# Kernel tuning notes

Measured on AMD Instinct MI355X. Metric: run time of the kernel, lower is better.

## Reference

```python
import jax, jax.numpy as jnp
import numpy as np

N = 100000      # nodes
E = 1600000     # directed edges (avg degree 16)
D_IN = 64
D_OUT = 64


def setup_inputs() -> dict:
    key = jax.random.key(0)
    k1, k2, k3, k4, k5 = jax.random.split(key, 5)
    x = jax.random.normal(k1, (N, D_IN), dtype=jnp.float32)
    edge_index = jax.random.randint(k2, (2, E), 0, N, dtype=jnp.int32)
    s_in = 1.0 / np.sqrt(D_IN)
    W_conv = jax.random.normal(k3, (D_IN, D_OUT), dtype=jnp.float32) * s_in
    b_conv = jnp.zeros((D_OUT,), dtype=jnp.float32)
    W_self = jax.random.normal(k4, (D_IN, D_OUT), dtype=jnp.float32) * s_in
    b_self = jax.random.normal(k5, (D_OUT,), dtype=jnp.float32) * s_in
    return {"x": x, "edge_index": edge_index, "W_conv": W_conv, "b_conv": b_conv,
            "W_self": W_self, "b_self": b_self, "n1": 400, "n2": 250}


def reference(x, edge_index, W_conv, b_conv, W_self, b_self, n1, n2):
    # GCNConv (PyG defaults): add self-loops, symmetric normalization,
    # out_i = sum_j norm_ij * (x_j @ W_conv) + b_conv; then self-loop linear + residual.
    n = x.shape[0]
    loops = jnp.arange(n, dtype=edge_index.dtype)
    row = jnp.concatenate([edge_index[0], loops])  # source nodes [E+N]
    col = jnp.concatenate([edge_index[1], loops])  # target nodes [E+N]
    deg = jax.ops.segment_sum(jnp.ones_like(col, dtype=x.dtype), col, num_segments=n)
    dinv = jnp.where(deg > 0, jax.lax.rsqrt(deg), 0.0)      # deg^{-1/2}
    norm = dinv[row] * dinv[col]                            # [E+N]
    xw = x @ W_conv                                         # [N, D_OUT]
    msg = xw[row] * norm[:, None]                           # gather + scale [E+N, D_OUT]
    x_neigh = jax.ops.segment_sum(msg, col, num_segments=n) + b_conv
    x_self = x @ W_self + b_self
    return x_self + x_neigh
```

## Files before the change

kernel.cpp:

```cpp
#include <hip/hip_runtime.h>

#define CAP 64
#define CHUNK 4096
#define NBINS_MAX 1024
#define CAPB 2560

typedef __attribute__((ext_vector_type(8))) short bf16x8;
typedef __attribute__((ext_vector_type(4))) float f32x4;

__device__ __forceinline__ unsigned short f2bf_rne(float f) {
    unsigned u = __builtin_bit_cast(unsigned, f);
    u += 0x7FFFu + ((u >> 16) & 1u);
    return (unsigned short)(u >> 16);
}
__device__ __forceinline__ float bf2f(unsigned short h) {
    return __builtin_bit_cast(float, (unsigned)h << 16);
}


__global__ void k_zero2(int* __restrict__ gcur, int nbins, int* __restrict__ degovf,
                        int n, int* __restrict__ ovfc,
                        const float* __restrict__ Wc, const float* __restrict__ Ws,
                        unsigned short* __restrict__ bfrag) {
    const int t = threadIdx.x;
    if (blockIdx.x == gridDim.x - 1) {
        for (int s = t; s < 2048; s += 256) {
            int lane = s & 63;
            int ct   = (s >> 6) & 3;
            int ks   = (s >> 8) & 1;
            int half = (s >> 9) & 1;
            int mat  = (s >> 10) & 1;
            const float* W = mat ? Ws : Wc;
            int d = ct * 16 + (lane & 15);
            int kbase = ks * 32 + (lane >> 4) * 8;
#pragma unroll
            for (int j = 0; j < 8; ++j) {
                float v = W[(kbase + j) * 64 + d];
                unsigned u = __builtin_bit_cast(unsigned, v);
                unsigned short hi = (unsigned short)(u >> 16);
                unsigned short elem;
                if (half == 0) {
                    elem = hi;
                } else {
                    float fh = __builtin_bit_cast(float, (unsigned)hi << 16);
                    float fl = v - fh;
                    elem = (unsigned short)(__builtin_bit_cast(unsigned, fl) >> 16);
                }
                bfrag[(size_t)s * 8 + j] = elem;
            }
        }
        return;
    }
    int i = blockIdx.x * blockDim.x + t;
    if (i < nbins) gcur[i] = 0;
    if (i < n) degovf[i] = 0;
    if (i == 0) *ovfc = 0;
}

__global__ __launch_bounds__(512) void k_bin(
    const int* __restrict__ row, const int* __restrict__ col, int e, int nbins,
    int* __restrict__ gcur, unsigned int* __restrict__ records,
    int* __restrict__ degovf, int* __restrict__ ovf, int* __restrict__ ovfc)
{
    __shared__ int hist[NBINS_MAX];
    __shared__ int lofs[NBINS_MAX];
    __shared__ int gadj[NBINS_MAX];
    __shared__ int tscan[512];
    __shared__ unsigned int stage[CHUNK];
    __shared__ unsigned short sbin[CHUNK];

    const int t = threadIdx.x;
    const int base = blockIdx.x * CHUNK;
    int cnt = e - base; if (cnt > CHUNK) cnt = CHUNK;
    if (cnt <= 0) return;

    for (int i = t; i < nbins; i += 512) hist[i] = 0;
    __syncthreads();

    for (int k = t; k < cnt; k += 512) atomicAdd(&hist[col[base + k] >> 7], 1);
    __syncthreads();

    const int b0 = t * 2;
    int h0 = (b0 < nbins) ? hist[b0] : 0;
    int h1 = (b0 + 1 < nbins) ? hist[b0 + 1] : 0;
    int s = h0 + h1;
    tscan[t] = s;
    __syncthreads();
    for (int off = 1; off < 512; off <<= 1) {
        int v = (t >= off) ? tscan[t - off] : 0;
        __syncthreads();
        tscan[t] += v;
        __syncthreads();
    }
    const int tbase = tscan[t] - s;

    if (b0 < nbins) {
        int gb = h0 ? atomicAdd(&gcur[b0], h0) : 0;
        lofs[b0] = tbase; gadj[b0] = gb - tbase;
    }
    if (b0 + 1 < nbins) {
        int lb = tbase + h0;
        int gb = h1 ? atomicAdd(&gcur[b0 + 1], h1) : 0;
        lofs[b0 + 1] = lb; gadj[b0 + 1] = gb - lb;
    }
    __syncthreads();

    for (int k = t; k < cnt; k += 512) {
        int c = col[base + k];
        int r = row[base + k];
        int b = c >> 7;
        int slot = atomicAdd(&lofs[b], 1);
        stage[slot] = ((unsigned)r << 7) | (unsigned)(c & 127);
        sbin[slot] = (unsigned short)b;
    }
    __syncthreads();

    for (int k = t; k < cnt; k += 512) {
        unsigned rec = stage[k];
        int b = sbin[k];
        int g = gadj[b] + k;
        if (g < CAPB) {
            records[(size_t)b * CAPB + g] = rec;
        } else {
            int q = atomicAdd(ovfc, 1);
            int c = (b << 7) | (int)(rec & 127u);
            ovf[2 * q]     = (int)(rec >> 7);
            ovf[2 * q + 1] = c;
            atomicAdd(&degovf[c], 1);
        }
    }
}

__global__ __launch_bounds__(256) void k_gemm6(
    const float* __restrict__ x, const unsigned short* __restrict__ bfrag,
    const float* __restrict__ bc, const float* __restrict__ bs,
    const unsigned int* __restrict__ records, const int* __restrict__ gcur,
    const int* __restrict__ degovf, float* __restrict__ dinv,
    unsigned short* __restrict__ ybf, float* __restrict__ out, int n)
{
    __shared__ int lh[128];
    __shared__ float sdinv[128];

    const int b = blockIdx.x;
    const int t = threadIdx.x;

    if (t < 128) lh[t] = 0;
    __syncthreads();
    int m = gcur[b]; if (m > CAPB) m = CAPB;
    const unsigned int* rb = records + (size_t)b * CAPB;
    for (int k = t; k < m; k += 256) atomicAdd(&lh[rb[k] & 127u], 1);
    __syncthreads();
    if (t < 128) {
        int node = (b << 7) + t;
        int dov = (node < n) ? degovf[node] : 0;
        float v = rsqrtf((float)(lh[t] + dov + 1));
        sdinv[t] = v;
        if (node < n) dinv[node] = v;
    }
    __syncthreads();

    const int lane = t & 63;
    const int wid = t >> 6;
    const int rt0 = b * 128 + wid * 32;
    const int lbase = wid * 32;
    if (rt0 >= n) return;

    const int arow = lane & 15;
    const int kgrp = lane >> 4;

    bf16x8 a_hi[2][2];
#pragma unroll
    for (int rt = 0; rt < 2; ++rt) {
        int row = rt0 + rt * 16 + arow;
        if (row >= n) row = n - 1;
        const float* xp = x + (size_t)row * 64 + kgrp * 8;
#pragma unroll
        for (int ks = 0; ks < 2; ++ks) {
            float4 f0 = *(const float4*)(xp + ks * 32);
            float4 f1 = *(const float4*)(xp + ks * 32 + 4);
            float f[8] = {f0.x, f0.y, f0.z, f0.w, f1.x, f1.y, f1.z, f1.w};
            bf16x8 h;
#pragma unroll
            for (int j = 0; j < 8; ++j) {
                unsigned u = __builtin_bit_cast(unsigned, f[j]);
                h[j] = (short)(unsigned short)(u >> 16);
            }
            a_hi[rt][ks] = h;
        }
    }

    f32x4 acc[2][2][4];
#pragma unroll
    for (int mm = 0; mm < 2; ++mm)
#pragma unroll
        for (int rt = 0; rt < 2; ++rt)
#pragma unroll
            for (int ct = 0; ct < 4; ++ct)
                acc[mm][rt][ct] = (f32x4){0.f, 0.f, 0.f, 0.f};

#pragma unroll
    for (int mat = 0; mat < 2; ++mat) {
#pragma unroll
        for (int ks = 0; ks < 2; ++ks) {
#pragma unroll
            for (int ct = 0; ct < 4; ++ct) {
                const bf16x8 bh = *(const bf16x8*)(bfrag + ((size_t)((((mat * 2 + 0) * 2 + ks) * 4 + ct) * 64 + lane)) * 8);
                const bf16x8 bl = *(const bf16x8*)(bfrag + ((size_t)((((mat * 2 + 1) * 2 + ks) * 4 + ct) * 64 + lane)) * 8);
#pragma unroll
                for (int rt = 0; rt < 2; ++rt) {
                    acc[mat][rt][ct] = __builtin_amdgcn_mfma_f32_16x16x32_bf16(a_hi[rt][ks], bh, acc[mat][rt][ct], 0, 0, 0);
                    acc[mat][rt][ct] = __builtin_amdgcn_mfma_f32_16x16x32_bf16(a_hi[rt][ks], bl, acc[mat][rt][ct], 0, 0, 0);
                }
            }
        }
    }

    const int dcol = lane & 15;
    const int rbase = (lane >> 4) * 4;
    float di[2][4];
#pragma unroll
    for (int rt = 0; rt < 2; ++rt)
#pragma unroll
        for (int reg = 0; reg < 4; ++reg)
            di[rt][reg] = sdinv[lbase + rt * 16 + rbase + reg];

#pragma unroll
    for (int ct = 0; ct < 4; ++ct) {
        int d = ct * 16 + dcol;
        float bias = bc[d] + bs[d];
#pragma unroll
        for (int rt = 0; rt < 2; ++rt) {
#pragma unroll
            for (int reg = 0; reg < 4; ++reg) {
                int row = rt0 + rt * 16 + rbase + reg;
                if (row < n) {
                    float dv = di[rt][reg];
                    float zc = acc[0][rt][ct][reg];
                    ybf[(size_t)row * 64 + d] = f2bf_rne(zc * dv);
                    out[(size_t)row * 64 + d] = acc[1][rt][ct][reg] + bias + dv * dv * zc;
                }
            }
        }
    }
}

__global__ __launch_bounds__(512) void k_gather_bin4(
    const int* __restrict__ gcur, const unsigned int* __restrict__ records,
    const unsigned short* __restrict__ ybf, const float* __restrict__ dinv,
    float* __restrict__ out, int n)
{
    __shared__ unsigned int srec[CAPB];
    __shared__ int slist[CAPB];
    __shared__ int scnt[128];
    __shared__ int sinc[128];
    __shared__ int scur[128];

    const int b = blockIdx.x, t = threadIdx.x;
    int m = gcur[b]; if (m > CAPB) m = CAPB;

    if (t < 128) scnt[t] = 0;
    __syncthreads();

    for (int k = t; k < m; k += 512) {
        unsigned r = __builtin_nontemporal_load(&records[(size_t)b * CAPB + k]);
        srec[k] = r;
        atomicAdd(&scnt[r & 127u], 1);
    }
    __syncthreads();

    if (t < 128) sinc[t] = scnt[t];
    __syncthreads();
    for (int off = 1; off < 128; off <<= 1) {
        int v = 0;
        if (t < 128 && t >= off) v = sinc[t - off];
        __syncthreads();
        if (t < 128) sinc[t] += v;
        __syncthreads();
    }
    if (t < 128) scur[t] = sinc[t] - scnt[t];
    __syncthreads();

    for (int k = t; k < m; k += 512) {
        unsigned r = srec[k];
        int slot = atomicAdd(&scur[r & 127u], 1);
        slist[slot] = (int)(r & ~127u);
    }
    __syncthreads();

    const int wave = t >> 6, lane = t & 63;
    const int h = lane >> 5;
    const char* ybl = (const char*)ybf + ((lane & 31) << 2);

    for (int i = wave; i < 128; i += 8) {
        int node = (b << 7) + i;
        if (node >= n) break;
        int cnt = scnt[i];
        if (cnt == 0) continue;
        int beg = sinc[i] - cnt;
        float ax0=0.f,ax1=0.f,ax2=0.f,ax3=0.f,ax4=0.f,ax5=0.f,ax6=0.f,ax7=0.f;
        float ay0=0.f,ay1=0.f,ay2=0.f,ay3=0.f,ay4=0.f,ay5=0.f,ay6=0.f,ay7=0.f;
        int k = 0;
        for (; k + 16 <= cnt; k += 16) {
            int o0 = slist[beg + k + 0  + h];
            int o1 = slist[beg + k + 2  + h];
            int o2 = slist[beg + k + 4  + h];
            int o3 = slist[beg + k + 6  + h];
            int o4 = slist[beg + k + 8  + h];
            int o5 = slist[beg + k + 10 + h];
            int o6 = slist[beg + k + 12 + h];
            int o7 = slist[beg + k + 14 + h];
            unsigned v0 = *(const unsigned*)(ybl + o0);
            unsigned v1 = *(const unsigned*)(ybl + o1);
            unsigned v2 = *(const unsigned*)(ybl + o2);
            unsigned v3 = *(const unsigned*)(ybl + o3);
            unsigned v4 = *(const unsigned*)(ybl + o4);
            unsigned v5 = *(const unsigned*)(ybl + o5);
            unsigned v6 = *(const unsigned*)(ybl + o6);
            unsigned v7 = *(const unsigned*)(ybl + o7);
            ax0 += bf2f((unsigned short)v0); ay0 += bf2f((unsigned short)(v0 >> 16));
            ax1 += bf2f((unsigned short)v1); ay1 += bf2f((unsigned short)(v1 >> 16));
            ax2 += bf2f((unsigned short)v2); ay2 += bf2f((unsigned short)(v2 >> 16));
            ax3 += bf2f((unsigned short)v3); ay3 += bf2f((unsigned short)(v3 >> 16));
            ax4 += bf2f((unsigned short)v4); ay4 += bf2f((unsigned short)(v4 >> 16));
            ax5 += bf2f((unsigned short)v5); ay5 += bf2f((unsigned short)(v5 >> 16));
            ax6 += bf2f((unsigned short)v6); ay6 += bf2f((unsigned short)(v6 >> 16));
            ax7 += bf2f((unsigned short)v7); ay7 += bf2f((unsigned short)(v7 >> 16));
        }
        for (; k + 2 <= cnt; k += 2) {
            int o = slist[beg + k + h];
            unsigned v = *(const unsigned*)(ybl + o);
            ax0 += bf2f((unsigned short)v);
            ay0 += bf2f((unsigned short)(v >> 16));
        }
        if (k < cnt && h == 0) {
            int o = slist[beg + k];
            unsigned v = *(const unsigned*)(ybl + o);
            ax0 += bf2f((unsigned short)v);
            ay0 += bf2f((unsigned short)(v >> 16));
        }
        float sx = ((ax0+ax1)+(ax2+ax3)) + ((ax4+ax5)+(ax6+ax7));
        float sy = ((ay0+ay1)+(ay2+ay3)) + ((ay4+ay5)+(ay6+ay7));
        sx += __shfl_down(sx, 32);
        sy += __shfl_down(sy, 32);
        if (h == 0) {
            float dv = dinv[node];
            float* op = out + (size_t)node * 64 + ((lane & 31) << 1);
            float p0 = __builtin_nontemporal_load(op);
            float p1 = __builtin_nontemporal_load(op + 1);
            __builtin_nontemporal_store(p0 + dv * sx, op);
            __builtin_nontemporal_store(p1 + dv * sy, op + 1);
        }
    }
}

__global__ void k_ovf2(const int* __restrict__ ovfc, const int* __restrict__ ovf,
                       const float* __restrict__ dinv, const unsigned short* __restrict__ ybf,
                       float* __restrict__ out) {
    int m = *ovfc;
    long long total = (long long)m * 64;
    for (long long idx = blockIdx.x * blockDim.x + threadIdx.x; idx < total;
         idx += (long long)gridDim.x * blockDim.x) {
        int q = (int)(idx >> 6);
        int j = (int)(idx & 63);
        int r = ovf[2 * q], c = ovf[2 * q + 1];
        float s = dinv[c];
        float v = bf2f(ybf[(size_t)r * 64 + j]);
        unsafeAtomicAdd(out + (size_t)c * 64 + j, s * v);
    }
}


__global__ void k_init(int* __restrict__ cnt, int* __restrict__ ovf_cnt, int n) {
    int i = blockIdx.x * blockDim.x + threadIdx.x;
    if (i < n) cnt[i] = 0;
    if (i == 0) *ovf_cnt = 0;
}

__global__ void k_fill_pad(const int* __restrict__ row, const int* __restrict__ col,
                           int* __restrict__ cnt, int* __restrict__ bucket,
                           int* __restrict__ ovf, int* __restrict__ ovf_cnt, int e) {
    int i = blockIdx.x * blockDim.x + threadIdx.x;
    if (i >= e) return;
    int c = col[i];
    int p = atomicAdd(&cnt[c], 1);
    if (p < CAP) bucket[(size_t)c * CAP + p] = row[i];
    else { int q = atomicAdd(ovf_cnt, 1); ovf[q] = i; }
}

__global__ __launch_bounds__(256) void k_gemm(
    const float* __restrict__ x, const float* __restrict__ Wc,
    const float* __restrict__ bc, const float* __restrict__ Ws,
    const float* __restrict__ bs, const int* __restrict__ deg, int add,
    float* __restrict__ dinv, float* __restrict__ y,
    float* __restrict__ out, int n)
{
    __shared__ __align__(16) float sWc[64 * 64];
    __shared__ __align__(16) float sWs[64 * 64];
    __shared__ __align__(16) float sx[64 * 64];
    const int t = threadIdx.x;

    for (int i = t; i < 1024; i += 256) {
        ((float4*)sWc)[i] = ((const float4*)Wc)[i];
        ((float4*)sWs)[i] = ((const float4*)Ws)[i];
    }
    const int row0 = blockIdx.x * 64;
    int nrows = n - row0; if (nrows > 64) nrows = 64;
    for (int i = t; i < nrows * 16; i += 256) {
        ((float4*)sx)[i] = ((const float4*)(x + (size_t)row0 * 64))[i];
    }
    __syncthreads();

    const int d = t & 63;
    const int g = t >> 6;

    float wcr[64], wsr[64];
#pragma unroll
    for (int k = 0; k < 64; ++k) { wcr[k] = sWc[k * 64 + d]; wsr[k] = sWs[k * 64 + d]; }

    const float bcd = bc[d], bsd = bs[d];

    for (int rr = g * 16; rr < (g + 1) * 16; ++rr) {
        if (rr >= nrows) break;
        float accC = 0.f, accS = 0.f;
        const float4* xv4 = (const float4*)(sx + rr * 64);
#pragma unroll
        for (int q = 0; q < 16; ++q) {
            float4 xv = xv4[q];
            accC += xv.x*wcr[4*q+0] + xv.y*wcr[4*q+1] + xv.z*wcr[4*q+2] + xv.w*wcr[4*q+3];
            accS += xv.x*wsr[4*q+0] + xv.y*wsr[4*q+1] + xv.z*wsr[4*q+2] + xv.w*wsr[4*q+3];
        }
        const int r = row0 + rr;
        const float di = rsqrtf((float)(deg[r] + add));
        if (d == 0) dinv[r] = di;
        const float yv = accC * di;
        y[(size_t)r * 64 + d] = yv;
        out[(size_t)r * 64 + d] = accS + bsd + bcd + di * yv;
    }
}

__global__ __launch_bounds__(256) void k_gather_pad(
    const int* __restrict__ cnt, const int* __restrict__ bucket,
    const float* __restrict__ y, float* __restrict__ out, int n)
{
    const int node = blockIdx.x * 4 + (threadIdx.x >> 6);
    if (node >= n) return;
    const int lane = threadIdx.x & 63;
    int m = cnt[node];
    const float di = rsqrtf((float)(m + 1));
    if (m > CAP) m = CAP;
    if (m == 0) return;

    int rl = (lane < m) ? bucket[(size_t)node * CAP + lane] : 0;

    float a0=0.f,a1=0.f,a2=0.f,a3=0.f,a4=0.f,a5=0.f,a6=0.f,a7=0.f;
    int k = 0;
    for (; k + 8 <= m; k += 8) {
        int r0=__shfl(rl,k+0), r1=__shfl(rl,k+1), r2=__shfl(rl,k+2), r3=__shfl(rl,k+3);
        int r4=__shfl(rl,k+4), r5=__shfl(rl,k+5), r6=__shfl(rl,k+6), r7=__shfl(rl,k+7);
        a0 += y[(size_t)r0*64 + lane];
        a1 += y[(size_t)r1*64 + lane];
        a2 += y[(size_t)r2*64 + lane];
        a3 += y[(size_t)r3*64 + lane];
        a4 += y[(size_t)r4*64 + lane];
        a5 += y[(size_t)r5*64 + lane];
        a6 += y[(size_t)r6*64 + lane];
        a7 += y[(size_t)r7*64 + lane];
    }
    for (; k + 2 <= m; k += 2) {
        int r0=__shfl(rl,k+0), r1=__shfl(rl,k+1);
        a0 += y[(size_t)r0*64 + lane];
        a1 += y[(size_t)r1*64 + lane];
    }
    if (k < m) { int r0=__shfl(rl,k); a0 += y[(size_t)r0*64 + lane]; }

    float acc = ((a0+a1)+(a2+a3)) + ((a4+a5)+(a6+a7));
    out[(size_t)node*64 + lane] += di * acc;
}

__global__ void k_ovf_idx(const int* __restrict__ ovf_cnt, const int* __restrict__ ovf,
                          const int* __restrict__ row, const int* __restrict__ col,
                          const float* __restrict__ dinv, const float* __restrict__ y,
                          float* __restrict__ out) {
    int m = *ovf_cnt;
    long long total = (long long)m * 16;
    for (long long idx = blockIdx.x*blockDim.x+threadIdx.x; idx < total;
         idx += (long long)gridDim.x*blockDim.x) {
        int ei = ovf[idx >> 4];
        int j = (int)(idx & 15);
        int r = row[ei], c = col[ei];
        float s = dinv[c];
        float4 v = ((const float4*)y)[(size_t)r*16 + j];
        float* o = out + (size_t)c*64 + (j<<2);
        unsafeAtomicAdd(o+0, s*v.x);
        unsafeAtomicAdd(o+1, s*v.y);
        unsafeAtomicAdd(o+2, s*v.z);
        unsafeAtomicAdd(o+3, s*v.w);
    }
}

__global__ void k_deg_init(int* __restrict__ deg, int n) {
    int i = blockIdx.x * blockDim.x + threadIdx.x;
    if (i < n) deg[i] = 1;
}

__global__ void k_deg_count(const int* __restrict__ col, int* __restrict__ deg, int e) {
    int i = blockIdx.x * blockDim.x + threadIdx.x;
    if (i < e) atomicAdd(&deg[col[i]], 1);
}

__global__ __launch_bounds__(256) void k_scatter(
    const int* __restrict__ row, const int* __restrict__ col,
    const float* __restrict__ dinv, const float* __restrict__ y,
    float* __restrict__ out, int e)
{
    int idx = blockIdx.x * blockDim.x + threadIdx.x;
    int eidx = idx >> 4;
    if (eidx >= e) return;
    int j = idx & 15;
    int r = row[eidx];
    int c = col[eidx];
    float s = dinv[c];
    float4 v = ((const float4*)y)[(size_t)r * 16 + j];
    float* o = out + (size_t)c * 64 + (j << 2);
    unsafeAtomicAdd(o + 0, s * v.x);
    unsafeAtomicAdd(o + 1, s * v.y);
    unsafeAtomicAdd(o + 2, s * v.z);
    unsafeAtomicAdd(o + 3, s * v.w);
}

extern "C" void kernel_launch(void* const* d_in, const int* in_sizes, int n_in,
                              void* d_out, int out_size, void* d_ws, size_t ws_size,
                              hipStream_t stream) {
    const float* x  = (const float*)d_in[0];
    const int*   ei = (const int*)d_in[1];
    const float* Wc = (const float*)d_in[2];
    const float* bc = (const float*)d_in[3];
    const float* Ws = (const float*)d_in[4];
    const float* bs = (const float*)d_in[5];
    float* out = (float*)d_out;

    const int n = in_sizes[0] / 64;
    const int e = in_sizes[1] / 2;
    const int* rowi = ei;
    const int* coli = ei + e;

    auto align = [](size_t v) { return (v + 255) & ~(size_t)255; };
    char* ws = (char*)d_ws;
    const int nbins = (n + 127) >> 7;

    size_t m_dinv = 0;
    size_t m_y    = align(m_dinv + (size_t)n * 4);
    size_t m_gcur = align(m_y    + (size_t)n * 128);
    size_t m_rec  = align(m_gcur + (size_t)nbins * 4);
    size_t m_dov  = align(m_rec  + (size_t)nbins * CAPB * 4);
    size_t m_ovf  = align(m_dov  + (size_t)n * 4);
    size_t m_ovfc = align(m_ovf  + (size_t)e * 8);
    size_t m_bfr  = align(m_ovfc + 256);
    size_t m_tot  = m_bfr + 32768;

    size_t p_cnt  = 0;
    size_t p_dinv = align(p_cnt  + (size_t)n * 4);
    size_t p_y    = align(p_dinv + (size_t)n * 4);
    size_t p_bkt  = align(p_y    + (size_t)n * 256);
    size_t p_ovf  = align(p_bkt  + (size_t)n * CAP * 4);
    size_t p_ovfc = align(p_ovf  + (size_t)e * 4);
    size_t p_tot  = p_ovfc + 256;

    if (nbins <= NBINS_MAX && m_tot <= ws_size) {
        float* dinv = (float*)(ws + m_dinv);
        unsigned short* ybf = (unsigned short*)(ws + m_y);
        int*   gcur = (int*)(ws + m_gcur);
        unsigned int* rec = (unsigned int*)(ws + m_rec);
        int*   dov  = (int*)(ws + m_dov);
        int*   ovf  = (int*)(ws + m_ovf);
        int*   ovfc = (int*)(ws + m_ovfc);
        unsigned short* bfrag = (unsigned short*)(ws + m_bfr);

        int zmax = (n > nbins) ? n : nbins;
        k_zero2<<<(zmax + 255) / 256 + 1, 256, 0, stream>>>(gcur, nbins, dov, n, ovfc,
                                                            Wc, Ws, bfrag);
        k_bin<<<(e + CHUNK - 1) / CHUNK, 512, 0, stream>>>(rowi, coli, e, nbins,
                                                           gcur, rec, dov, ovf, ovfc);
        k_gemm6<<<nbins, 256, 0, stream>>>(x, bfrag, bc, bs, rec, gcur, dov,
                                           dinv, ybf, out, n);
        k_gather_bin4<<<nbins, 512, 0, stream>>>(gcur, rec, ybf, dinv, out, n);
        k_ovf2<<<64, 256, 0, stream>>>(ovfc, ovf, dinv, ybf, out);
    } else if (p_tot <= ws_size) {
        int*   cnt    = (int*)(ws + p_cnt);
        float* dinv   = (float*)(ws + p_dinv);
        float* y      = (float*)(ws + p_y);
        int*   bucket = (int*)(ws + p_bkt);
        int*   ovf    = (int*)(ws + p_ovf);
        int*   ovfc   = (int*)(ws + p_ovfc);

        k_init<<<(n + 255) / 256, 256, 0, stream>>>(cnt, ovfc, n);
        k_fill_pad<<<(e + 255) / 256, 256, 0, stream>>>(rowi, coli, cnt, bucket, ovf, ovfc, e);
        k_gemm<<<(n + 63) / 64, 256, 0, stream>>>(x, Wc, bc, Ws, bs, cnt, 1, dinv, y, out, n);
        k_gather_pad<<<(n + 3) / 4, 256, 0, stream>>>(cnt, bucket, y, out, n);
        k_ovf_idx<<<64, 256, 0, stream>>>(ovfc, ovf, rowi, coli, dinv, y, out);
    } else {
        size_t a_deg  = 0;
        size_t a_dinv = align(a_deg  + (size_t)n * 4);
        size_t a_y    = align(a_dinv + (size_t)n * 4);
        int*   deg  = (int*)(ws + a_deg);
        float* dinv = (float*)(ws + a_dinv);
        float* y    = (float*)(ws + a_y);
        k_deg_init<<<(n + 255) / 256, 256, 0, stream>>>(deg, n);
        k_deg_count<<<(e + 255) / 256, 256, 0, stream>>>(coli, deg, e);
        k_gemm<<<(n + 63) / 64, 256, 0, stream>>>(x, Wc, bc, Ws, bs, deg, 0, dinv, y, out, n);
        long long tot = (long long)e * 16;
        k_scatter<<<(int)((tot + 255) / 256), 256, 0, stream>>>(rowi, coli, dinv, y, out, e);
    }
}
```

Baseline: 113.9 us.

## Aggregate dinv-scaled bf16 features before the GEMM instead of after

Reorders the GCN computation so neighbours' dinv-scaled bf16 inputs are aggregated first, and a single fused GEMM then applies W_conv to the aggregate and W_self to x. This avoids the read-modify-write of the fp32 output in the gather kernel, and the separate ybf plus out writes from the first GEMM. In exchange it adds a prep kernel, an extra bf16 aggregate buffer and a fourth launch. The overflow path now does a per-edge 64x64 matvec, and rounding the aggregate to bf16 before the GEMM may change numerical error.

```diff
diff --git a/kernel.cpp b/kernel.cpp
--- a/kernel.cpp
+++ b/kernel.cpp
@@ -131,18 +131,14 @@
     }
 }
 
-__global__ __launch_bounds__(256) void k_gemm6(
-    const float* __restrict__ x, const unsigned short* __restrict__ bfrag,
-    const float* __restrict__ bc, const float* __restrict__ bs,
-    const unsigned int* __restrict__ records, const int* __restrict__ gcur,
-    const int* __restrict__ degovf, float* __restrict__ dinv,
-    unsigned short* __restrict__ ybf, float* __restrict__ out, int n)
+__global__ __launch_bounds__(256) void k_xprep(
+    const float* __restrict__ x, const unsigned int* __restrict__ records,
+    const int* __restrict__ gcur, const int* __restrict__ degovf,
+    float* __restrict__ dinv, unsigned short* __restrict__ xbf, int n)
 {
     __shared__ int lh[128];
     __shared__ float sdinv[128];
-
-    const int b = blockIdx.x;
-    const int t = threadIdx.x;
+    const int b = blockIdx.x, t = threadIdx.x;
 
     if (t < 128) lh[t] = 0;
     __syncthreads();
@@ -159,95 +155,26 @@
     }
     __syncthreads();
 
-    const int lane = t & 63;
-    const int wid = t >> 6;
-    const int rt0 = b * 128 + wid * 32;
-    const int lbase = wid * 32;
-    if (rt0 >= n) return;
-
-    const int arow = lane & 15;
-    const int kgrp = lane >> 4;
-
-    bf16x8 a_hi[2][2];
-#pragma unroll
-    for (int rt = 0; rt < 2; ++rt) {
-        int row = rt0 + rt * 16 + arow;
-        if (row >= n) row = n - 1;
-        const float* xp = x + (size_t)row * 64 + kgrp * 8;
-#pragma unroll
-        for (int ks = 0; ks < 2; ++ks) {
-            float4 f0 = *(const float4*)(xp + ks * 32);
-            float4 f1 = *(const float4*)(xp + ks * 32 + 4);
-            float f[8] = {f0.x, f0.y, f0.z, f0.w, f1.x, f1.y, f1.z, f1.w};
-            bf16x8 h;
-#pragma unroll
-            for (int j = 0; j < 8; ++j) {
-                unsigned u = __builtin_bit_cast(unsigned, f[j]);
-                h[j] = (short)(unsigned short)(u >> 16);
-            }
-            a_hi[rt][ks] = h;
-        }
-    }
-
-    f32x4 acc[2][2][4];
-#pragma unroll
-    for (int mm = 0; mm < 2; ++mm)
-#pragma unroll
-        for (int rt = 0; rt < 2; ++rt)
-#pragma unroll
-            for (int ct = 0; ct < 4; ++ct)
-                acc[mm][rt][ct] = (f32x4){0.f, 0.f, 0.f, 0.f};
-
-#pragma unroll
-    for (int mat = 0; mat < 2; ++mat) {
-#pragma unroll
-        for (int ks = 0; ks < 2; ++ks) {
-#pragma unroll
-            for (int ct = 0; ct < 4; ++ct) {
-                const bf16x8 bh = *(const bf16x8*)(bfrag + ((size_t)((((mat * 2 + 0) * 2 + ks) * 4 + ct) * 64 + lane)) * 8);
-                const bf16x8 bl = *(const bf16x8*)(bfrag + ((size_t)((((mat * 2 + 1) * 2 + ks) * 4 + ct) * 64 + lane)) * 8);
-#pragma unroll
-                for (int rt = 0; rt < 2; ++rt) {
-                    acc[mat][rt][ct] = __builtin_amdgcn_mfma_f32_16x16x32_bf16(a_hi[rt][ks], bh, acc[mat][rt][ct], 0, 0, 0);
-                    acc[mat][rt][ct] = __builtin_amdgcn_mfma_f32_16x16x32_bf16(a_hi[rt][ks], bl, acc[mat][rt][ct], 0, 0, 0);
-                }
-            }
-        }
-    }
-
-    const int dcol = lane & 15;
-    const int rbase = (lane >> 4) * 4;
-    float di[2][4];
-#pragma unroll
-    for (int rt = 0; rt < 2; ++rt)
-#pragma unroll
-        for (int reg = 0; reg < 4; ++reg)
-            di[rt][reg] = sdinv[lbase + rt * 16 + rbase + reg];
-
-#pragma unroll
-    for (int ct = 0; ct < 4; ++ct) {
-        int d = ct * 16 + dcol;
-        float bias = bc[d] + bs[d];
-#pragma unroll
-        for (int rt = 0; rt < 2; ++rt) {
-#pragma unroll
-            for (int reg = 0; reg < 4; ++reg) {
-                int row = rt0 + rt * 16 + rbase + reg;
-                if (row < n) {
-                    float dv = di[rt][reg];
-                    float zc = acc[0][rt][ct][reg];
-                    ybf[(size_t)row * 64 + d] = f2bf_rne(zc * dv);
-                    out[(size_t)row * 64 + d] = acc[1][rt][ct][reg] + bias + dv * dv * zc;
-                }
-            }
-        }
-    }
-}
-
-__global__ __launch_bounds__(512) void k_gather_bin4(
+#pragma unroll
+    for (int i = 0; i < 4; ++i) {
+        int pos = t + i * 256;
+        int node = (b << 7) + (pos >> 3);
+        if (node >= n) break;
+        float dv = sdinv[pos >> 3];
+        const float4* xp = (const float4*)(x + (size_t)b * 8192 + (size_t)pos * 8);
+        float4 f0 = xp[0], f1 = xp[1];
+        uint4 u;
+        u.x = (unsigned)f2bf_rne(f0.x * dv) | ((unsigned)f2bf_rne(f0.y * dv) << 16);
+        u.y = (unsigned)f2bf_rne(f0.z * dv) | ((unsigned)f2bf_rne(f0.w * dv) << 16);
+        u.z = (unsigned)f2bf_rne(f1.x * dv) | ((unsigned)f2bf_rne(f1.y * dv) << 16);
+        u.w = (unsigned)f2bf_rne(f1.z * dv) | ((unsigned)f2bf_rne(f1.w * dv) << 16);
+        *(uint4*)(xbf + (size_t)b * 8192 + (size_t)pos * 8) = u;
+    }
+}
+
+__global__ __launch_bounds__(512) void k_agg(
     const int* __restrict__ gcur, const unsigned int* __restrict__ records,
-    const unsigned short* __restrict__ ybf, const float* __restrict__ dinv,
-    float* __restrict__ out, int n)
+    const unsigned short* __restrict__ xbf, unsigned short* __restrict__ agg, int n)
 {
     __shared__ unsigned int srec[CAPB];
     __shared__ int slist[CAPB];
@@ -289,13 +216,12 @@
 
     const int wave = t >> 6, lane = t & 63;
     const int h = lane >> 5;
-    const char* ybl = (const char*)ybf + ((lane & 31) << 2);
+    const char* ybl = (const char*)xbf + ((lane & 31) << 2);
 
     for (int i = wave; i < 128; i += 8) {
         int node = (b << 7) + i;
         if (node >= n) break;
         int cnt = scnt[i];
-        if (cnt == 0) continue;
         int beg = sinc[i] - cnt;
         float ax0=0.f,ax1=0.f,ax2=0.f,ax3=0.f,ax4=0.f,ax5=0.f,ax6=0.f,ax7=0.f;
         float ay0=0.f,ay1=0.f,ay2=0.f,ay3=0.f,ay4=0.f,ay5=0.f,ay6=0.f,ay7=0.f;
@@ -343,29 +269,129 @@
         sx += __shfl_down(sx, 32);
         sy += __shfl_down(sy, 32);
         if (h == 0) {
-            float dv = dinv[node];
-            float* op = out + (size_t)node * 64 + ((lane & 31) << 1);
-            float p0 = __builtin_nontemporal_load(op);
-            float p1 = __builtin_nontemporal_load(op + 1);
-            __builtin_nontemporal_store(p0 + dv * sx, op);
-            __builtin_nontemporal_store(p1 + dv * sy, op + 1);
-        }
-    }
-}
-
-__global__ void k_ovf2(const int* __restrict__ ovfc, const int* __restrict__ ovf,
-                       const float* __restrict__ dinv, const unsigned short* __restrict__ ybf,
-                       float* __restrict__ out) {
+            unsigned own = *(const unsigned*)((const char*)xbf + ((size_t)node << 7) + ((lane & 31) << 2));
+            sx += bf2f((unsigned short)own);
+            sy += bf2f((unsigned short)(own >> 16));
+            unsigned pk = (unsigned)f2bf_rne(sx) | ((unsigned)f2bf_rne(sy) << 16);
+            __builtin_nontemporal_store(pk,
+                (unsigned*)((char*)agg + ((size_t)node << 7) + ((lane & 31) << 2)));
+        }
+    }
+}
+
+__global__ __launch_bounds__(256) void k_gemm7(
+    const float* __restrict__ x, const unsigned short* __restrict__ aggbf,
+    const unsigned short* __restrict__ bfrag, const float* __restrict__ bc,
+    const float* __restrict__ bs, const float* __restrict__ dinv,
+    float* __restrict__ out, int n)
+{
+    __shared__ float sdinv[128];
+    const int b = blockIdx.x;
+    const int t = threadIdx.x;
+    if (t < 128) {
+        int node = (b << 7) + t;
+        sdinv[t] = (node < n) ? dinv[node] : 0.f;
+    }
+    __syncthreads();
+
+    const int lane = t & 63;
+    const int wid = t >> 6;
+    const int rt0 = b * 128 + wid * 32;
+    const int lbase = wid * 32;
+    if (rt0 >= n) return;
+
+    const int arow = lane & 15;
+    const int kgrp = lane >> 4;
+
+    bf16x8 a_x[2][2], a_g[2][2];
+#pragma unroll
+    for (int rt = 0; rt < 2; ++rt) {
+        int row = rt0 + rt * 16 + arow;
+        if (row >= n) row = n - 1;
+        const float* xp = x + (size_t)row * 64 + kgrp * 8;
+#pragma unroll
+        for (int ks = 0; ks < 2; ++ks) {
+            float4 f0 = *(const float4*)(xp + ks * 32);
+            float4 f1 = *(const float4*)(xp + ks * 32 + 4);
+            float f[8] = {f0.x, f0.y, f0.z, f0.w, f1.x, f1.y, f1.z, f1.w};
+            bf16x8 hh;
+#pragma unroll
+            for (int j = 0; j < 8; ++j) {
+                unsigned u = __builtin_bit_cast(unsigned, f[j]);
+                hh[j] = (short)(unsigned short)(u >> 16);
+            }
+            a_x[rt][ks] = hh;
+            a_g[rt][ks] = *(const bf16x8*)(aggbf + (size_t)row * 64 + ks * 32 + kgrp * 8);
+        }
+    }
+
+    f32x4 acc[2][2][4];
+#pragma unroll
+    for (int mm = 0; mm < 2; ++mm)
+#pragma unroll
+        for (int rt = 0; rt < 2; ++rt)
+#pragma unroll
+            for (int ct = 0; ct < 4; ++ct)
+                acc[mm][rt][ct] = (f32x4){0.f, 0.f, 0.f, 0.f};
+
+#pragma unroll
+    for (int mat = 0; mat < 2; ++mat) {
+#pragma unroll
+        for (int ks = 0; ks < 2; ++ks) {
+#pragma unroll
+            for (int ct = 0; ct < 4; ++ct) {
+                const bf16x8 bh = *(const bf16x8*)(bfrag + ((size_t)((((mat * 2 + 0) * 2 + ks) * 4 + ct) * 64 + lane)) * 8);
+                const bf16x8 bl = *(const bf16x8*)(bfrag + ((size_t)((((mat * 2 + 1) * 2 + ks) * 4 + ct) * 64 + lane)) * 8);
+#pragma unroll
+                for (int rt = 0; rt < 2; ++rt) {
+                    bf16x8 A = (mat == 0) ? a_g[rt][ks] : a_x[rt][ks];
+                    acc[mat][rt][ct] = __builtin_amdgcn_mfma_f32_16x16x32_bf16(A, bh, acc[mat][rt][ct], 0, 0, 0);
+                    acc[mat][rt][ct] = __builtin_amdgcn_mfma_f32_16x16x32_bf16(A, bl, acc[mat][rt][ct], 0, 0, 0);
+                }
+            }
+        }
+    }
+
+    const int dcol = lane & 15;
+    const int rbase = (lane >> 4) * 4;
+    float di[2][4];
+#pragma unroll
+    for (int rt = 0; rt < 2; ++rt)
+#pragma unroll
+        for (int reg = 0; reg < 4; ++reg)
+            di[rt][reg] = sdinv[lbase + rt * 16 + rbase + reg];
+
+#pragma unroll
+    for (int ct = 0; ct < 4; ++ct) {
+        int d = ct * 16 + dcol;
+        float bias = bc[d] + bs[d];
+#pragma unroll
+        for (int rt = 0; rt < 2; ++rt) {
+#pragma unroll
+            for (int reg = 0; reg < 4; ++reg) {
+                int row = rt0 + rt * 16 + rbase + reg;
+                if (row < n) {
+                    out[(size_t)row * 64 + d] =
+                        acc[1][rt][ct][reg] + bias + di[rt][reg] * acc[0][rt][ct][reg];
+                }
+            }
+        }
+    }
+}
+
+__global__ void k_ovf3(const int* __restrict__ ovfc, const int* __restrict__ ovf,
+                       const float* __restrict__ dinv, const unsigned short* __restrict__ xbf,
+                       const float* __restrict__ Wc, float* __restrict__ out) {
     int m = *ovfc;
-    long long total = (long long)m * 64;
-    for (long long idx = blockIdx.x * blockDim.x + threadIdx.x; idx < total;
-         idx += (long long)gridDim.x * blockDim.x) {
-        int q = (int)(idx >> 6);
-        int j = (int)(idx & 63);
+    int wid = (blockIdx.x * blockDim.x + threadIdx.x) >> 6;
+    int lane = threadIdx.x & 63;
+    int nw = (gridDim.x * blockDim.x) >> 6;
+    for (int q = wid; q < m; q += nw) {
         int r = ovf[2 * q], c = ovf[2 * q + 1];
-        float s = dinv[c];
-        float v = bf2f(ybf[(size_t)r * 64 + j]);
-        unsafeAtomicAdd(out + (size_t)c * 64 + j, s * v);
+        float acc = 0.f;
+        for (int k = 0; k < 64; ++k)
+            acc += bf2f(xbf[(size_t)r * 64 + k]) * Wc[k * 64 + lane];
+        unsafeAtomicAdd(out + (size_t)c * 64 + lane, dinv[c] * acc);
     }
 }
 
@@ -549,8 +575,9 @@
     const int nbins = (n + 127) >> 7;
 
     size_t m_dinv = 0;
-    size_t m_y    = align(m_dinv + (size_t)n * 4);
-    size_t m_gcur = align(m_y    + (size_t)n * 128);
+    size_t m_xbf  = align(m_dinv + (size_t)n * 4);
+    size_t m_agg  = align(m_xbf  + (size_t)n * 128);
+    size_t m_gcur = align(m_agg  + (size_t)n * 128);
     size_t m_rec  = align(m_gcur + (size_t)nbins * 4);
     size_t m_dov  = align(m_rec  + (size_t)nbins * CAPB * 4);
     size_t m_ovf  = align(m_dov  + (size_t)n * 4);
@@ -568,7 +595,8 @@
 
     if (nbins <= NBINS_MAX && m_tot <= ws_size) {
         float* dinv = (float*)(ws + m_dinv);
-        unsigned short* ybf = (unsigned short*)(ws + m_y);
+        unsigned short* xbf = (unsigned short*)(ws + m_xbf);
+        unsigned short* agg = (unsigned short*)(ws + m_agg);
         int*   gcur = (int*)(ws + m_gcur);
         unsigned int* rec = (unsigned int*)(ws + m_rec);
         int*   dov  = (int*)(ws + m_dov);
@@ -581,10 +609,10 @@
                                                             Wc, Ws, bfrag);
         k_bin<<<(e + CHUNK - 1) / CHUNK, 512, 0, stream>>>(rowi, coli, e, nbins,
                                                            gcur, rec, dov, ovf, ovfc);
-        k_gemm6<<<nbins, 256, 0, stream>>>(x, bfrag, bc, bs, rec, gcur, dov,
-                                           dinv, ybf, out, n);
-        k_gather_bin4<<<nbins, 512, 0, stream>>>(gcur, rec, ybf, dinv, out, n);
-        k_ovf2<<<64, 256, 0, stream>>>(ovfc, ovf, dinv, ybf, out);
+        k_xprep<<<nbins, 256, 0, stream>>>(x, rec, gcur, dov, dinv, xbf, n);
+        k_agg<<<nbins, 512, 0, stream>>>(gcur, rec, xbf, agg, n);
+        k_gemm7<<<nbins, 256, 0, stream>>>(x, agg, bfrag, bc, bs, dinv, out, n);
+        k_ovf3<<<64, 256, 0, stream>>>(ovfc, ovf, dinv, xbf, Wc, out);
     } else if (p_tot <= ws_size) {
         int*   cnt    = (int*)(ws + p_cnt);
         float* dinv   = (float*)(ws + p_dinv);
```

Measured after the change: 115.1 us. Within noise of the previous version (+1.1%).
